# Kernel optimization log

Measured on AMD Instinct MI355X. Metric: run time of the kernel, lower is better.

The kernel has to match this reference:

```python
import jax, jax.numpy as jnp
import numpy as np

D_MODEL = 1024
N_HEAD = 16
HEAD_DIM = D_MODEL // N_HEAD
B, L = 2, 2048


def setup_inputs() -> dict:
    key = jax.random.key(0)
    ks = jax.random.split(key, 5)
    std = 1.0 / np.sqrt(D_MODEL)
    x = jax.random.normal(ks[0], (B, L, D_MODEL), dtype=jnp.float32)
    # nn.MultiheadAttention packed in-projection: [3*D, D] weight, [3*D] bias
    in_proj_w = jax.random.normal(ks[1], (3 * D_MODEL, D_MODEL), dtype=jnp.float32) * std
    in_proj_b = jax.random.normal(ks[2], (3 * D_MODEL,), dtype=jnp.float32) * 0.01
    out_w = jax.random.normal(ks[3], (D_MODEL, D_MODEL), dtype=jnp.float32) * std
    out_b = jax.random.normal(ks[4], (D_MODEL,), dtype=jnp.float32) * 0.01
    return {"x": x, "in_proj_w": in_proj_w, "in_proj_b": in_proj_b,
            "out_w": out_w, "out_b": out_b}


def reference(x, in_proj_w, in_proj_b, out_w, out_b):
    b, l, d = x.shape
    h, dh = N_HEAD, HEAD_DIM
    # packed QKV projection: [B,L,3D]
    qkv = jnp.einsum('bld,ed->ble', x, in_proj_w) + in_proj_b
    q, k, v = jnp.split(qkv, 3, axis=-1)
    # [B,H,L,dh]
    q = q.reshape(b, l, h, dh).transpose(0, 2, 1, 3)
    k = k.reshape(b, l, h, dh).transpose(0, 2, 1, 3)
    v = v.reshape(b, l, h, dh).transpose(0, 2, 1, 3)
    scale = 1.0 / jnp.sqrt(jnp.asarray(dh, dtype=x.dtype))
    scores = jnp.einsum('bhqd,bhkd->bhqk', q, k) * scale  # [B,H,L,L]
    causal = jnp.tril(jnp.ones((l, l), dtype=bool))
    scores = jnp.where(causal, scores, jnp.asarray(-jnp.inf, dtype=scores.dtype))
    attn = jax.nn.softmax(scores, axis=-1)
    ctx = jnp.einsum('bhqk,bhkd->bhqd', attn, v)  # [B,H,L,dh]
    ctx = ctx.transpose(0, 2, 1, 3).reshape(b, l, d)
    out = jnp.einsum('bld,ed->ble', ctx, out_w) + out_b
    return out
```

## Files before the change

kernel.cpp:

```cpp
#include <hip/hip_runtime.h>
#include <hip/hip_bf16.h>

typedef __attribute__((ext_vector_type(8))) short short8;
typedef __attribute__((ext_vector_type(4))) short short4v;
typedef __attribute__((ext_vector_type(4))) float f32x4;

#define GAS(p) ((const __attribute__((address_space(1))) void*)(p))
#define LAS(p) ((__attribute__((address_space(3))) void*)(p))

__device__ __forceinline__ short f2bf_bits(float f) {
    __hip_bfloat16 h = __float2bfloat16(f);
    return *reinterpret_cast<short*>(&h);
}

__global__ __launch_bounds__(256) void cvt_bf16(const float* __restrict__ src,
                                                short* __restrict__ dst, int n) {
    int i = (blockIdx.x * 256 + threadIdx.x) * 8;
    if (i >= n) return;
    float4 a = *reinterpret_cast<const float4*>(src + i);
    float4 b = *reinterpret_cast<const float4*>(src + i + 4);
    short8 o;
    o[0] = f2bf_bits(a.x); o[1] = f2bf_bits(a.y);
    o[2] = f2bf_bits(a.z); o[3] = f2bf_bits(a.w);
    o[4] = f2bf_bits(b.x); o[5] = f2bf_bits(b.y);
    o[6] = f2bf_bits(b.z); o[7] = f2bf_bits(b.w);
    *reinterpret_cast<short8*>(dst + i) = o;
}

__global__ __launch_bounds__(256) void gemm_qkv(const __hip_bfloat16* __restrict__ A,
                                                const __hip_bfloat16* __restrict__ B,
                                                const float* __restrict__ bias,
                                                __hip_bfloat16* __restrict__ Qb,
                                                __hip_bfloat16* __restrict__ Kb,
                                                __hip_bfloat16* __restrict__ Vb) {
    constexpr int K = 1024;
    __shared__ __hip_bfloat16 smem[2][128 * 32 + 128 * 32];
    const int tid = threadIdx.x;
    const int lane = tid & 63, wid = tid >> 6;
    const int wr = wid >> 1, wc = wid & 1;
    const int lr = lane & 15, lg = lane >> 4;
    const int m0 = blockIdx.y * 128;
    const int n0 = blockIdx.x * 128;

    const f32x4 fz = {0.f, 0.f, 0.f, 0.f};
    f32x4 acc[4][4];
#pragma unroll
    for (int i = 0; i < 4; i++)
#pragma unroll
        for (int j = 0; j < 4; j++) acc[i][j] = fz;

    const char* Abase = (const char*)A + (size_t)m0 * K * 2;
    const char* Bbase = (const char*)B + (size_t)n0 * K * 2;

    auto stage = [&](int buf, int kt) {
        const int kb = kt * 64;
        char* sA = (char*)&smem[buf][0];
        char* sB = (char*)&smem[buf][128 * 32];
#pragma unroll
        for (int i = 0; i < 2; i++) {
            int o = i * 4096 + tid * 16;
            int row = o >> 6, cb = o & 63;
            __builtin_amdgcn_global_load_lds(GAS(Abase + (size_t)row * 2048 + kb + cb),
                                             LAS(sA + o), 16, 0, 0);
        }
#pragma unroll
        for (int i = 0; i < 2; i++) {
            int o = i * 4096 + tid * 16;
            int row = o >> 6, cb = o & 63;
            __builtin_amdgcn_global_load_lds(GAS(Bbase + (size_t)row * 2048 + kb + cb),
                                             LAS(sB + o), 16, 0, 0);
        }
    };

    stage(0, 0);
    __syncthreads();
    int buf = 0;
    constexpr int NT = K / 32;
    for (int kt = 0; kt < NT; ++kt) {
        if (kt + 1 < NT) stage(buf ^ 1, kt + 1);
        const __hip_bfloat16* sA = &smem[buf][0];
        const __hip_bfloat16* sB = &smem[buf][128 * 32];
        short8 a[4], b[4];
#pragma unroll
        for (int i = 0; i < 4; i++)
            a[i] = *reinterpret_cast<const short8*>(sA + (wr * 64 + i * 16 + lr) * 32 + lg * 8);
#pragma unroll
        for (int j = 0; j < 4; j++)
            b[j] = *reinterpret_cast<const short8*>(sB + (wc * 64 + j * 16 + lr) * 32 + lg * 8);
#pragma unroll
        for (int i = 0; i < 4; i++)
#pragma unroll
            for (int j = 0; j < 4; j++)
                acc[i][j] = __builtin_amdgcn_mfma_f32_16x16x32_bf16(a[i], b[j], acc[i][j], 0, 0, 0);
        __syncthreads();
        buf ^= 1;
    }

#pragma unroll
    for (int j = 0; j < 4; j++) {
        int e = n0 + wc * 64 + j * 16 + lr;
        float bv = bias[e];
        int sec = e >> 10;
        int el = e & 1023;
        int h = el >> 6, d = el & 63;
        __hip_bfloat16* dst = (sec == 0) ? Qb : ((sec == 1) ? Kb : Vb);
        float scale = (sec == 0) ? 0.125f : 1.0f;
#pragma unroll
        for (int i = 0; i < 4; i++) {
            int mb = m0 + wr * 64 + i * 16 + lg * 4;
#pragma unroll
            for (int r = 0; r < 4; r++) {
                int tok = mb + r;
                int bb = tok >> 11, l = tok & 2047;
                float v = (acc[i][j][r] + bv) * scale;
                dst[((size_t)(bb * 16 + h) * 2048 + l) * 64 + d] = __float2bfloat16(v);
            }
        }
    }
}

__global__ __launch_bounds__(256) void transpose_v(const __hip_bfloat16* __restrict__ V,
                                                   __hip_bfloat16* __restrict__ Vt) {
    __shared__ unsigned short tb[64][72];
    int bh = blockIdx.y, l0 = blockIdx.x * 64;
    int tid = threadIdx.x;
    const unsigned short* src = (const unsigned short*)V + ((size_t)bh * 2048 + l0) * 64;
#pragma unroll
    for (int i = 0; i < 2; i++) {
        int idx = i * 256 + tid;
        int row = idx >> 3;
        int c0 = (idx & 7) * 8;
        short8 v = *reinterpret_cast<const short8*>(src + row * 64 + c0);
#pragma unroll
        for (int jj = 0; jj < 8; jj++) tb[c0 + jj][row] = (unsigned short)v[jj];
    }
    __syncthreads();
    unsigned short* dst = (unsigned short*)Vt + (size_t)bh * 64 * 2048 + l0;
#pragma unroll
    for (int i = 0; i < 2; i++) {
        int idx = i * 256 + tid;
        int d = idx >> 3;
        int c8 = (idx & 7) * 8;
        short8 vv = *reinterpret_cast<const short8*>(&tb[d][c8]);
        *reinterpret_cast<short8*>(dst + (size_t)d * 2048 + c8) = vv;
    }
}

__global__ __launch_bounds__(256) void attn(const __hip_bfloat16* __restrict__ Qg,
                                            const __hip_bfloat16* __restrict__ Kg,
                                            const __hip_bfloat16* __restrict__ Vtg,
                                            __hip_bfloat16* __restrict__ ctx) {
    const int bh = blockIdx.y;
    const int tid = threadIdx.x, lane = tid & 63, wq = tid >> 6;
    const int lr = lane & 15, lg = lane >> 4;

    __shared__ __hip_bfloat16 Ks[2][64 * 64];
    __shared__ __hip_bfloat16 Vs[2][64 * 64];
    __shared__ __hip_bfloat16 Ps[4][16 * 72];

    const char* kbase = (const char*)Kg + (size_t)bh * 2048 * 64 * 2;
    const char* vbase = (const char*)Vtg + (size_t)bh * 64 * 2048 * 2;
    const int bb = bh >> 4, h = bh & 15;

    auto stage = [&](int buf, int kt) {
        int kv0 = kt * 64;
        char* sK = (char*)&Ks[buf][0];
        char* sV = (char*)&Vs[buf][0];
#pragma unroll
        for (int i = 0; i < 2; i++) {
            int o_ = i * 4096 + tid * 16;
            int row = o_ >> 7;
            int slot = (o_ >> 4) & 7;
            int sl = slot ^ (row & 7);
            __builtin_amdgcn_global_load_lds(
                GAS(kbase + ((size_t)(kv0 + row) * 64) * 2 + sl * 16), LAS(sK + o_), 16, 0, 0);
        }
#pragma unroll
        for (int i = 0; i < 2; i++) {
            int o_ = i * 4096 + tid * 16;
            int row = o_ >> 7;
            int slot = (o_ >> 4) & 7;
            int sl = slot ^ (row & 7);
            __builtin_amdgcn_global_load_lds(
                GAS(vbase + ((size_t)row * 2048 + kv0) * 2 + sl * 16), LAS(sV + o_), 16, 0, 0);
        }
    };

    const f32x4 fz = {0.f, 0.f, 0.f, 0.f};

#pragma unroll 1
    for (int seg = 0; seg < 2; ++seg) {
        const int qt = (seg == 0) ? (int)blockIdx.x : 31 - (int)blockIdx.x;
        const int qb = qt * 64 + wq * 16;

        const __hip_bfloat16* Qrow = Qg + ((size_t)bh * 2048 + qb + lr) * 64 + lg * 8;
        short8 qf0 = *reinterpret_cast<const short8*>(Qrow);
        short8 qf1 = *reinterpret_cast<const short8*>(Qrow + 32);

        f32x4 o[4];
#pragma unroll
        for (int n = 0; n < 4; n++) o[n] = fz;
        float m = -1e30f, lsum = 0.f;

        const int NT = qt + 1;
        stage(0, 0);
        __syncthreads();
        int buf = 0;
        for (int kt = 0; kt < NT; ++kt) {
            if (kt + 1 < NT) stage(buf ^ 1, kt + 1);
            const __hip_bfloat16* sK = &Ks[buf][0];
            const __hip_bfloat16* sV = &Vs[buf][0];

            f32x4 s[4];
#pragma unroll
            for (int n = 0; n < 4; n++) s[n] = fz;
#pragma unroll
            for (int n = 0; n < 4; n++) {
                int kv = n * 16 + lr;
                short8 k0 = *reinterpret_cast<const short8*>(sK + kv * 64 + ((lg ^ (kv & 7)) * 8));
                short8 k1 = *reinterpret_cast<const short8*>(sK + kv * 64 + (((4 + lg) ^ (kv & 7)) * 8));
                s[n] = __builtin_amdgcn_mfma_f32_16x16x32_bf16(k0, qf0, s[n], 0, 0, 0);
                s[n] = __builtin_amdgcn_mfma_f32_16x16x32_bf16(k1, qf1, s[n], 0, 0, 0);
            }
            if (kt == NT - 1) {
                int q = qb + lr;
#pragma unroll
                for (int n = 0; n < 4; n++) {
                    int kvb = kt * 64 + n * 16 + lg * 4;
#pragma unroll
                    for (int r = 0; r < 4; r++)
                        if (kvb + r > q) s[n][r] = -1e30f;
                }
            }
            float mx0 = fmaxf(fmaxf(s[0][0], s[0][1]), fmaxf(s[0][2], s[0][3]));
            float mx1 = fmaxf(fmaxf(s[1][0], s[1][1]), fmaxf(s[1][2], s[1][3]));
            float mx2 = fmaxf(fmaxf(s[2][0], s[2][1]), fmaxf(s[2][2], s[2][3]));
            float mx3 = fmaxf(fmaxf(s[3][0], s[3][1]), fmaxf(s[3][2], s[3][3]));
            float mx = fmaxf(fmaxf(mx0, mx1), fmaxf(mx2, mx3));
            mx = fmaxf(mx, __shfl_xor(mx, 16));
            mx = fmaxf(mx, __shfl_xor(mx, 32));
            float mnew = fmaxf(m, mx);
            float corr = __expf(m - mnew);
            m = mnew;
            float ps = 0.f;
#pragma unroll
            for (int n = 0; n < 4; n++) {
#pragma unroll
                for (int r = 0; r < 4; r++) {
                    float p = __expf(s[n][r] - mnew);
                    s[n][r] = p;
                    ps += p;
                }
            }
            ps += __shfl_xor(ps, 16);
            ps += __shfl_xor(ps, 32);
            lsum = lsum * corr + ps;

            float c0 = __shfl(corr, (lane & 48) | ((lg * 4 + 0) & 15));
            float c1 = __shfl(corr, (lane & 48) | ((lg * 4 + 1) & 15));
            float c2 = __shfl(corr, (lane & 48) | ((lg * 4 + 2) & 15));
            float c3 = __shfl(corr, (lane & 48) | ((lg * 4 + 3) & 15));
#pragma unroll
            for (int n = 0; n < 4; n++) {
                o[n][0] *= c0; o[n][1] *= c1; o[n][2] *= c2; o[n][3] *= c3;
            }

            __hip_bfloat16* pw = &Ps[wq][0];
#pragma unroll
            for (int n = 0; n < 4; n++) {
                short4v pk;
                pk[0] = f2bf_bits(s[n][0]); pk[1] = f2bf_bits(s[n][1]);
                pk[2] = f2bf_bits(s[n][2]); pk[3] = f2bf_bits(s[n][3]);
                *reinterpret_cast<short4v*>(pw + lr * 72 + n * 16 + lg * 4) = pk;
            }
            asm volatile("s_waitcnt lgkmcnt(0)" ::: "memory");
            short8 pa0 = *reinterpret_cast<const short8*>(pw + lr * 72 + lg * 8);
            short8 pa1 = *reinterpret_cast<const short8*>(pw + lr * 72 + 32 + lg * 8);

#pragma unroll
            for (int n = 0; n < 4; n++) {
                int d = n * 16 + lr;
                short8 vf0 = *reinterpret_cast<const short8*>(sV + d * 64 + ((lg ^ (d & 7)) * 8));
                short8 vf1 = *reinterpret_cast<const short8*>(sV + d * 64 + (((4 + lg) ^ (d & 7)) * 8));
                o[n] = __builtin_amdgcn_mfma_f32_16x16x32_bf16(pa0, vf0, o[n], 0, 0, 0);
                o[n] = __builtin_amdgcn_mfma_f32_16x16x32_bf16(pa1, vf1, o[n], 0, 0, 0);
            }
            __syncthreads();
            buf ^= 1;
        }

        float l0 = __shfl(lsum, (lane & 48) | ((lg * 4 + 0) & 15));
        float l1 = __shfl(lsum, (lane & 48) | ((lg * 4 + 1) & 15));
        float l2 = __shfl(lsum, (lane & 48) | ((lg * 4 + 2) & 15));
        float l3 = __shfl(lsum, (lane & 48) | ((lg * 4 + 3) & 15));
        float inv[4] = {1.0f / l0, 1.0f / l1, 1.0f / l2, 1.0f / l3};
#pragma unroll
        for (int r = 0; r < 4; r++) {
            int tok = qb + lg * 4 + r;
            __hip_bfloat16* crow = ctx + ((size_t)(bb * 2048 + tok)) * 1024 + h * 64;
#pragma unroll
            for (int n = 0; n < 4; n++) crow[n * 16 + lr] = __float2bfloat16(o[n][r] * inv[r]);
        }
    }
}

__global__ __launch_bounds__(256) void gemm_out(const __hip_bfloat16* __restrict__ A,
                                                const __hip_bfloat16* __restrict__ B,
                                                const float* __restrict__ bias,
                                                float* __restrict__ out) {
    constexpr int K = 1024;
    __shared__ __hip_bfloat16 smem[2][128 * 32 + 64 * 32];
    const int tid = threadIdx.x;
    const int lane = tid & 63, wid = tid >> 6;
    const int wr = wid >> 1, wc = wid & 1;
    const int lr = lane & 15, lg = lane >> 4;
    const int m0 = blockIdx.y * 128;
    const int n0 = blockIdx.x * 64;

    const f32x4 fz = {0.f, 0.f, 0.f, 0.f};
    f32x4 acc[4][2];
#pragma unroll
    for (int i = 0; i < 4; i++)
#pragma unroll
        for (int j = 0; j < 2; j++) acc[i][j] = fz;

    const char* Abase = (const char*)A + (size_t)m0 * K * 2;
    const char* Bbase = (const char*)B + (size_t)n0 * K * 2;

    auto stage = [&](int buf, int kt) {
        const int kb = kt * 64;
        char* sA = (char*)&smem[buf][0];
        char* sB = (char*)&smem[buf][128 * 32];
#pragma unroll
        for (int i = 0; i < 2; i++) {
            int o = i * 4096 + tid * 16;
            int row = o >> 6, cb = o & 63;
            __builtin_amdgcn_global_load_lds(GAS(Abase + (size_t)row * 2048 + kb + cb),
                                             LAS(sA + o), 16, 0, 0);
        }
        {
            int o = tid * 16;
            int row = o >> 6, cb = o & 63;
            __builtin_amdgcn_global_load_lds(GAS(Bbase + (size_t)row * 2048 + kb + cb),
                                             LAS(sB + o), 16, 0, 0);
        }
    };

    stage(0, 0);
    __syncthreads();
    int buf = 0;
    constexpr int NT = K / 32;
    for (int kt = 0; kt < NT; ++kt) {
        if (kt + 1 < NT) stage(buf ^ 1, kt + 1);
        const __hip_bfloat16* sA = &smem[buf][0];
        const __hip_bfloat16* sB = &smem[buf][128 * 32];
        short8 a[4], b[2];
#pragma unroll
        for (int i = 0; i < 4; i++)
            a[i] = *reinterpret_cast<const short8*>(sA + (wr * 64 + i * 16 + lr) * 32 + lg * 8);
#pragma unroll
        for (int j = 0; j < 2; j++)
            b[j] = *reinterpret_cast<const short8*>(sB + (wc * 32 + j * 16 + lr) * 32 + lg * 8);
#pragma unroll
        for (int i = 0; i < 4; i++)
#pragma unroll
            for (int j = 0; j < 2; j++)
                acc[i][j] = __builtin_amdgcn_mfma_f32_16x16x32_bf16(a[i], b[j], acc[i][j], 0, 0, 0);
        __syncthreads();
        buf ^= 1;
    }

#pragma unroll
    for (int j = 0; j < 2; j++) {
        int e = n0 + wc * 32 + j * 16 + lr;
        float bv = bias[e];
#pragma unroll
        for (int i = 0; i < 4; i++) {
            int mb = m0 + wr * 64 + i * 16 + lg * 4;
#pragma unroll
            for (int r = 0; r < 4; r++) {
                out[(size_t)(mb + r) * 1024 + e] = acc[i][j][r] + bv;
            }
        }
    }
}

extern "C" void kernel_launch(void* const* d_in, const int* in_sizes, int n_in,
                              void* d_out, int out_size, void* d_ws, size_t ws_size,
                              hipStream_t stream) {
    const float* x = (const float*)d_in[0];
    const float* w_in = (const float*)d_in[1];
    const float* b_in = (const float*)d_in[2];
    const float* w_out = (const float*)d_in[3];
    const float* b_out = (const float*)d_in[4];
    float* out = (float*)d_out;

    char* ws = (char*)d_ws;
    __hip_bfloat16* xbf  = (__hip_bfloat16*)(ws);
    __hip_bfloat16* wbf  = (__hip_bfloat16*)(ws + (8ull << 20));
    __hip_bfloat16* owbf = (__hip_bfloat16*)(ws + (14ull << 20));
    __hip_bfloat16* Qb   = (__hip_bfloat16*)(ws + (16ull << 20));
    __hip_bfloat16* Kb   = (__hip_bfloat16*)(ws + (24ull << 20));
    __hip_bfloat16* Vb   = (__hip_bfloat16*)(ws + (32ull << 20));
    __hip_bfloat16* Vt   = (__hip_bfloat16*)(ws + (40ull << 20));
    __hip_bfloat16* ctxb = (__hip_bfloat16*)(ws + (48ull << 20));

    cvt_bf16<<<2048, 256, 0, stream>>>(x, (short*)xbf, 4194304);
    cvt_bf16<<<1536, 256, 0, stream>>>(w_in, (short*)wbf, 3145728);
    cvt_bf16<<<512, 256, 0, stream>>>(w_out, (short*)owbf, 1048576);
    gemm_qkv<<<dim3(24, 32), 256, 0, stream>>>(xbf, wbf, b_in, Qb, Kb, Vb);
    transpose_v<<<dim3(32, 32), 256, 0, stream>>>(Vb, Vt);
    attn<<<dim3(16, 32), 256, 0, stream>>>(Qb, Kb, Vt, ctxb);
    gemm_out<<<dim3(16, 32), 256, 0, stream>>>(ctxb, owbf, b_out, out);
}
```

Baseline: 199.5 us.

## Merge conversion kernels, use exp2 softmax with lazy rescale, and precompute attention offsets

Replaces the three bf16 conversion launches with a single kernel that routes by index range. Folds log2(e) into the Q scale so softmax can use exp2, and skips the output and sum rescaling when the running max has not grown past a threshold. Hoists the swizzled LDS and global staging offsets out of the inner attention loop, and raises wave priority around the MFMA blocks. The lazy rescale lets exp2 arguments grow up to the threshold before correction, which slightly loosens numeric headroom.

```diff
diff --git a/kernel.cpp b/kernel.cpp
--- a/kernel.cpp
+++ b/kernel.cpp
@@ -13,18 +13,26 @@
     return *reinterpret_cast<short*>(&h);
 }
 
-__global__ __launch_bounds__(256) void cvt_bf16(const float* __restrict__ src,
-                                                short* __restrict__ dst, int n) {
+__global__ __launch_bounds__(256) void cvt_all(const float* __restrict__ x,
+                                               const float* __restrict__ w1,
+                                               const float* __restrict__ w2,
+                                               short* __restrict__ dx,
+                                               short* __restrict__ dw1,
+                                               short* __restrict__ dw2) {
+    constexpr int N1 = 4194304, N2 = 3145728;
     int i = (blockIdx.x * 256 + threadIdx.x) * 8;
-    if (i >= n) return;
-    float4 a = *reinterpret_cast<const float4*>(src + i);
-    float4 b = *reinterpret_cast<const float4*>(src + i + 4);
+    const float* src; short* dst; int j;
+    if (i < N1)            { src = x;  dst = dx;  j = i; }
+    else if (i < N1 + N2)  { src = w1; dst = dw1; j = i - N1; }
+    else                   { src = w2; dst = dw2; j = i - N1 - N2; }
+    float4 a = *reinterpret_cast<const float4*>(src + j);
+    float4 b = *reinterpret_cast<const float4*>(src + j + 4);
     short8 o;
     o[0] = f2bf_bits(a.x); o[1] = f2bf_bits(a.y);
     o[2] = f2bf_bits(a.z); o[3] = f2bf_bits(a.w);
     o[4] = f2bf_bits(b.x); o[5] = f2bf_bits(b.y);
     o[6] = f2bf_bits(b.z); o[7] = f2bf_bits(b.w);
-    *reinterpret_cast<short8*>(dst + i) = o;
+    *reinterpret_cast<short8*>(dst + j) = o;
 }
 
 __global__ __launch_bounds__(256) void gemm_qkv(const __hip_bfloat16* __restrict__ A,
@@ -104,7 +112,7 @@
         int el = e & 1023;
         int h = el >> 6, d = el & 63;
         __hip_bfloat16* dst = (sec == 0) ? Qb : ((sec == 1) ? Kb : Vb);
-        float scale = (sec == 0) ? 0.125f : 1.0f;
+        float scale = (sec == 0) ? 0.18033688011112042f : 1.0f;
 #pragma unroll
         for (int i = 0; i < 4; i++) {
             int mb = m0 + wr * 64 + i * 16 + lg * 4;
@@ -158,32 +166,29 @@
     __shared__ __hip_bfloat16 Vs[2][64 * 64];
     __shared__ __hip_bfloat16 Ps[4][16 * 72];
 
-    const char* kbase = (const char*)Kg + (size_t)bh * 2048 * 64 * 2;
-    const char* vbase = (const char*)Vtg + (size_t)bh * 64 * 2048 * 2;
+    const char* kbase = (const char*)Kg + (size_t)bh * (2048 * 64 * 2);
+    const char* vbase = (const char*)Vtg + (size_t)bh * (64 * 2048 * 2);
     const int bb = bh >> 4, h = bh & 15;
 
+    const int srow = tid >> 3;
+    const int ssl = (tid & 7) ^ (srow & 7);
+    const char* gk0 = kbase + srow * 128 + ssl * 16;
+    const char* gv0 = vbase + (size_t)srow * 4096 + ssl * 16;
+
+    const int koffA = lr * 64 + ((lg ^ (lr & 7)) * 8);
+    const int koffB = lr * 64 + (((4 + lg) ^ (lr & 7)) * 8);
+    __hip_bfloat16* pwW = &Ps[wq][0] + lr * 72 + lg * 4;
+    const __hip_bfloat16* pwR = &Ps[wq][0] + lr * 72 + lg * 8;
+
     auto stage = [&](int buf, int kt) {
-        int kv0 = kt * 64;
-        char* sK = (char*)&Ks[buf][0];
-        char* sV = (char*)&Vs[buf][0];
-#pragma unroll
-        for (int i = 0; i < 2; i++) {
-            int o_ = i * 4096 + tid * 16;
-            int row = o_ >> 7;
-            int slot = (o_ >> 4) & 7;
-            int sl = slot ^ (row & 7);
-            __builtin_amdgcn_global_load_lds(
-                GAS(kbase + ((size_t)(kv0 + row) * 64) * 2 + sl * 16), LAS(sK + o_), 16, 0, 0);
-        }
-#pragma unroll
-        for (int i = 0; i < 2; i++) {
-            int o_ = i * 4096 + tid * 16;
-            int row = o_ >> 7;
-            int slot = (o_ >> 4) & 7;
-            int sl = slot ^ (row & 7);
-            __builtin_amdgcn_global_load_lds(
-                GAS(vbase + ((size_t)row * 2048 + kv0) * 2 + sl * 16), LAS(sV + o_), 16, 0, 0);
-        }
+        char* dK = (char*)&Ks[buf][0] + tid * 16;
+        char* dV = (char*)&Vs[buf][0] + tid * 16;
+        const char* srcK = gk0 + (size_t)kt * 8192;
+        const char* srcV = gv0 + (size_t)kt * 128;
+        __builtin_amdgcn_global_load_lds(GAS(srcK), LAS(dK), 16, 0, 0);
+        __builtin_amdgcn_global_load_lds(GAS(srcK + 4096), LAS(dK + 4096), 16, 0, 0);
+        __builtin_amdgcn_global_load_lds(GAS(srcV), LAS(dV), 16, 0, 0);
+        __builtin_amdgcn_global_load_lds(GAS(srcV + 131072), LAS(dV + 4096), 16, 0, 0);
     };
 
     const f32x4 fz = {0.f, 0.f, 0.f, 0.f};
@@ -214,14 +219,16 @@
             f32x4 s[4];
 #pragma unroll
             for (int n = 0; n < 4; n++) s[n] = fz;
+            __builtin_amdgcn_s_setprio(1);
 #pragma unroll
             for (int n = 0; n < 4; n++) {
-                int kv = n * 16 + lr;
-                short8 k0 = *reinterpret_cast<const short8*>(sK + kv * 64 + ((lg ^ (kv & 7)) * 8));
-                short8 k1 = *reinterpret_cast<const short8*>(sK + kv * 64 + (((4 + lg) ^ (kv & 7)) * 8));
+                short8 k0 = *reinterpret_cast<const short8*>(sK + koffA + n * 1024);
+                short8 k1 = *reinterpret_cast<const short8*>(sK + koffB + n * 1024);
                 s[n] = __builtin_amdgcn_mfma_f32_16x16x32_bf16(k0, qf0, s[n], 0, 0, 0);
                 s[n] = __builtin_amdgcn_mfma_f32_16x16x32_bf16(k1, qf1, s[n], 0, 0, 0);
             }
+            __builtin_amdgcn_s_setprio(0);
+
             if (kt == NT - 1) {
                 int q = qb + lr;
 #pragma unroll
@@ -232,67 +239,71 @@
                         if (kvb + r > q) s[n][r] = -1e30f;
                 }
             }
-            float mx0 = fmaxf(fmaxf(s[0][0], s[0][1]), fmaxf(s[0][2], s[0][3]));
-            float mx1 = fmaxf(fmaxf(s[1][0], s[1][1]), fmaxf(s[1][2], s[1][3]));
-            float mx2 = fmaxf(fmaxf(s[2][0], s[2][1]), fmaxf(s[2][2], s[2][3]));
-            float mx3 = fmaxf(fmaxf(s[3][0], s[3][1]), fmaxf(s[3][2], s[3][3]));
-            float mx = fmaxf(fmaxf(mx0, mx1), fmaxf(mx2, mx3));
+
+            float mx = fmaxf(fmaxf(fmaxf(s[0][0], s[0][1]), fmaxf(s[0][2], s[0][3])),
+                             fmaxf(fmaxf(fmaxf(s[1][0], s[1][1]), fmaxf(s[1][2], s[1][3])),
+                                   fmaxf(fmaxf(fmaxf(s[2][0], s[2][1]), fmaxf(s[2][2], s[2][3])),
+                                         fmaxf(fmaxf(s[3][0], s[3][1]), fmaxf(s[3][2], s[3][3])))));
             mx = fmaxf(mx, __shfl_xor(mx, 16));
             mx = fmaxf(mx, __shfl_xor(mx, 32));
-            float mnew = fmaxf(m, mx);
-            float corr = __expf(m - mnew);
-            m = mnew;
-            float ps = 0.f;
+
+            if (!__all(mx - m <= 11.54f)) {
+                float mnew = fmaxf(m, mx);
+                float corr = __builtin_amdgcn_exp2f(m - mnew);
+                m = mnew;
+                lsum *= corr;
+                float c0 = __shfl(corr, (lane & 48) | (lg * 4 + 0));
+                float c1 = __shfl(corr, (lane & 48) | (lg * 4 + 1));
+                float c2 = __shfl(corr, (lane & 48) | (lg * 4 + 2));
+                float c3 = __shfl(corr, (lane & 48) | (lg * 4 + 3));
+#pragma unroll
+                for (int n = 0; n < 4; n++) {
+                    o[n][0] *= c0; o[n][1] *= c1; o[n][2] *= c2; o[n][3] *= c3;
+                }
+            }
+
+            float psum = 0.f;
 #pragma unroll
             for (int n = 0; n < 4; n++) {
-#pragma unroll
-                for (int r = 0; r < 4; r++) {
-                    float p = __expf(s[n][r] - mnew);
-                    s[n][r] = p;
-                    ps += p;
-                }
-            }
-            ps += __shfl_xor(ps, 16);
-            ps += __shfl_xor(ps, 32);
-            lsum = lsum * corr + ps;
-
-            float c0 = __shfl(corr, (lane & 48) | ((lg * 4 + 0) & 15));
-            float c1 = __shfl(corr, (lane & 48) | ((lg * 4 + 1) & 15));
-            float c2 = __shfl(corr, (lane & 48) | ((lg * 4 + 2) & 15));
-            float c3 = __shfl(corr, (lane & 48) | ((lg * 4 + 3) & 15));
-#pragma unroll
-            for (int n = 0; n < 4; n++) {
-                o[n][0] *= c0; o[n][1] *= c1; o[n][2] *= c2; o[n][3] *= c3;
-            }
-
-            __hip_bfloat16* pw = &Ps[wq][0];
+                float p0 = __builtin_amdgcn_exp2f(s[n][0] - m);
+                float p1 = __builtin_amdgcn_exp2f(s[n][1] - m);
+                float p2 = __builtin_amdgcn_exp2f(s[n][2] - m);
+                float p3 = __builtin_amdgcn_exp2f(s[n][3] - m);
+                s[n][0] = p0; s[n][1] = p1; s[n][2] = p2; s[n][3] = p3;
+                psum += (p0 + p1) + (p2 + p3);
+            }
+            psum += __shfl_xor(psum, 16);
+            psum += __shfl_xor(psum, 32);
+            lsum += psum;
+
 #pragma unroll
             for (int n = 0; n < 4; n++) {
                 short4v pk;
                 pk[0] = f2bf_bits(s[n][0]); pk[1] = f2bf_bits(s[n][1]);
                 pk[2] = f2bf_bits(s[n][2]); pk[3] = f2bf_bits(s[n][3]);
-                *reinterpret_cast<short4v*>(pw + lr * 72 + n * 16 + lg * 4) = pk;
+                *reinterpret_cast<short4v*>(pwW + n * 16) = pk;
             }
             asm volatile("s_waitcnt lgkmcnt(0)" ::: "memory");
-            short8 pa0 = *reinterpret_cast<const short8*>(pw + lr * 72 + lg * 8);
-            short8 pa1 = *reinterpret_cast<const short8*>(pw + lr * 72 + 32 + lg * 8);
-
+            short8 pa0 = *reinterpret_cast<const short8*>(pwR);
+            short8 pa1 = *reinterpret_cast<const short8*>(pwR + 32);
+
+            __builtin_amdgcn_s_setprio(1);
 #pragma unroll
             for (int n = 0; n < 4; n++) {
-                int d = n * 16 + lr;
-                short8 vf0 = *reinterpret_cast<const short8*>(sV + d * 64 + ((lg ^ (d & 7)) * 8));
-                short8 vf1 = *reinterpret_cast<const short8*>(sV + d * 64 + (((4 + lg) ^ (d & 7)) * 8));
+                short8 vf0 = *reinterpret_cast<const short8*>(sV + koffA + n * 1024);
+                short8 vf1 = *reinterpret_cast<const short8*>(sV + koffB + n * 1024);
                 o[n] = __builtin_amdgcn_mfma_f32_16x16x32_bf16(pa0, vf0, o[n], 0, 0, 0);
                 o[n] = __builtin_amdgcn_mfma_f32_16x16x32_bf16(pa1, vf1, o[n], 0, 0, 0);
             }
+            __builtin_amdgcn_s_setprio(0);
             __syncthreads();
             buf ^= 1;
         }
 
-        float l0 = __shfl(lsum, (lane & 48) | ((lg * 4 + 0) & 15));
-        float l1 = __shfl(lsum, (lane & 48) | ((lg * 4 + 1) & 15));
-        float l2 = __shfl(lsum, (lane & 48) | ((lg * 4 + 2) & 15));
-        float l3 = __shfl(lsum, (lane & 48) | ((lg * 4 + 3) & 15));
+        float l0 = __shfl(lsum, (lane & 48) | (lg * 4 + 0));
+        float l1 = __shfl(lsum, (lane & 48) | (lg * 4 + 1));
+        float l2 = __shfl(lsum, (lane & 48) | (lg * 4 + 2));
+        float l3 = __shfl(lsum, (lane & 48) | (lg * 4 + 3));
         float inv[4] = {1.0f / l0, 1.0f / l1, 1.0f / l2, 1.0f / l3};
 #pragma unroll
         for (int r = 0; r < 4; r++) {
@@ -405,9 +416,7 @@
     __hip_bfloat16* Vt   = (__hip_bfloat16*)(ws + (40ull << 20));
     __hip_bfloat16* ctxb = (__hip_bfloat16*)(ws + (48ull << 20));
 
-    cvt_bf16<<<2048, 256, 0, stream>>>(x, (short*)xbf, 4194304);
-    cvt_bf16<<<1536, 256, 0, stream>>>(w_in, (short*)wbf, 3145728);
-    cvt_bf16<<<512, 256, 0, stream>>>(w_out, (short*)owbf, 1048576);
+    cvt_all<<<4096, 256, 0, stream>>>(x, w_in, w_out, (short*)xbf, (short*)wbf, (short*)owbf);
     gemm_qkv<<<dim3(24, 32), 256, 0, stream>>>(xbf, wbf, b_in, Qb, Kb, Vb);
     transpose_v<<<dim3(32, 32), 256, 0, stream>>>(Vb, Vt);
     attn<<<dim3(16, 32), 256, 0, stream>>>(Qb, Kb, Vt, ctxb);
```

After: 192.7 us. 1.03x faster.
